# Kernel tuning notes

Hardware: AMD Instinct MI355X
Metric: run time of the kernel (lower is better)

## Reference

```python
import jax, jax.numpy as jnp
import numpy as np

HEAD_NUM = 6

def setup_inputs() -> dict:
    key = jax.random.key(0)
    k1, k2, k3 = jax.random.split(key, 3)
    B, N, P, C = 4, 64, 256, 384
    x = jax.random.normal(k1, (B, N, P, C), dtype=jnp.float32)
    # torch Linear init scale ~ 1/sqrt(fan_in); keep magnitudes sane
    w_qkv = jax.random.normal(k2, (C, 3 * C), dtype=jnp.float32) * (1.0 / np.sqrt(C))
    w_proj = jax.random.normal(k3, (C, C), dtype=jnp.float32) * (1.0 / np.sqrt(C))
    b_proj = jnp.zeros((C,), dtype=jnp.float32)
    return {"x": x, "w_qkv": w_qkv, "w_proj": w_proj, "b_proj": b_proj}

def reference(x, w_qkv, w_proj, b_proj):
    B, N, P, C = x.shape
    H = HEAD_NUM
    D = C // H
    scale = jnp.asarray(D, dtype=x.dtype)  # NOTE: head_dim ** 1, faithful to source
    qkv = (x @ w_qkv).reshape(B, N, P, 3, H, D)
    q = qkv[:, :, :, 0]  # (B, N, P, H, D)
    k = qkv[:, :, :, 1]
    v = qkv[:, :, :, 2]
    attn = jnp.einsum('bnphd,bnqhd->bnhpq', q, k) * scale  # (B,N,H,P,P)
    attn = jax.nn.softmax(attn, axis=-1)
    out = jnp.einsum('bnhpq,bnqhd->bnphd', attn, v).reshape(B, N, P, C)
    return out @ w_proj + b_proj
```

## Files before the change

### kernel.cpp

```cpp
#include <hip/hip_runtime.h>

typedef __bf16 bf16_t;
typedef __bf16 bf16x8 __attribute__((ext_vector_type(8)));
typedef float f32x4 __attribute__((ext_vector_type(4)));
typedef unsigned short u16;
typedef unsigned short u16x4 __attribute__((ext_vector_type(4)));
typedef unsigned int u32;

#define B_ 4
#define N_ 64
#define P_ 256
#define C_ 384
#define H_ 6
#define D_ 64
#define M_TOTAL 65536
#define NQKV 1152
#define KSTEPS 12
#define NFRAG 12
#define WF_HSTRIDE (KSTEPS*NFRAG*512)
#define NBLK (H_*B_*N_)
#define FUSED_LDS 139264
#define PB_STRIDE 40
#define SB() __builtin_amdgcn_sched_barrier(0)

__device__ __forceinline__ u16 f2b(float f){ return __builtin_bit_cast(u16, (bf16_t)f); }
__device__ __forceinline__ f32x4 mfma(bf16x8 a, bf16x8 b, f32x4 c){
    return __builtin_amdgcn_mfma_f32_16x16x32_bf16(a, b, c, 0, 0, 0);
}

__global__ __launch_bounds__(256) void prep_w(
    const float* __restrict__ wqkv, const float* __restrict__ wproj,
    u16* __restrict__ Wfh, u16* __restrict__ Wfl, u16* __restrict__ wPt)
{
    int i = blockIdx.x * 256 + threadIdx.x;
    const int NSLOT = H_ * KSTEPS * NFRAG * 64;
    if (i < NSLOT) {
        int lane = i & 63;
        int frag = i >> 6;
        int nf = frag % NFRAG;
        int ks = (frag / NFRAG) % KSTEPS;
        int h  = frag / (NFRAG * KSTEPS);
        int part = nf >> 2;
        int nh   = (nf & 3) * 16 + (lane & 15);
        int col  = part * C_ + h * 64 + nh;
        int k0   = ks * 32 + (lane >> 4) * 8;
        #pragma unroll
        for (int e = 0; e < 8; ++e) {
            float w = wqkv[(size_t)(k0 + e) * NQKV + col];
            bf16_t hi = (bf16_t)w;
            Wfh[(size_t)i * 8 + e] = __builtin_bit_cast(u16, hi);
            Wfl[(size_t)i * 8 + e] = f2b(w - (float)hi);
        }
    }
    int j = i - NSLOT;
    if (j >= 0 && j < C_ * C_) {
        int k = j / C_, n = j % C_;
        wPt[(size_t)n * C_ + k] = f2b(wproj[j]);
    }
}

__global__ __launch_bounds__(512)
__attribute__((amdgpu_waves_per_eu(2, 2)))
void fused_attn(
    const float* __restrict__ x, const u16* __restrict__ Wfh,
    const u16* __restrict__ Wfl, u16* __restrict__ attn)
{
    extern __shared__ u16 sm[];
    u16* Kh = sm;
    u16* Kl = sm + 16384;
    u16* Vt = sm + 32768;
    u16* Qb = sm + 49152;

    const int tid  = threadIdx.x;
    const int lane = tid & 63, wid = tid >> 6;
    const int g = lane >> 4, r16 = lane & 15;

    const int p = blockIdx.x;
    const int logical = (p & 7) * (NBLK / 8) + (p >> 3);
    const int h  = logical % H_;
    const int bn = logical / H_;
    const size_t row0 = (size_t)bn * P_;
    const int m0w = wid * 32;

    f32x4 acc[2][12];
    #pragma unroll
    for (int mf = 0; mf < 2; ++mf)
        #pragma unroll
        for (int nf = 0; nf < 12; ++nf) acc[mf][nf] = f32x4{0.f,0.f,0.f,0.f};

    const float* xr0 = x + (row0 + m0w + r16) * C_;
    const float* xr1 = xr0 + 16 * C_;
    const u16* wh = Wfh + (size_t)h * WF_HSTRIDE + lane * 8;
    const u16* wl = Wfl + (size_t)h * WF_HSTRIDE + lane * 8;

    bf16x8 bhv[2][12];
    bf16x8 blv[2][8];
    bf16x8 ahq[2][2], alq[2][2];
    f32x4 xr[4];

#define SPLIT_A(par) do {                                                    \
    _Pragma("unroll")                                                        \
    for (int e = 0; e < 4; ++e) {                                            \
        bf16_t h0 = (bf16_t)xr[0][e], h1 = (bf16_t)xr[1][e];                 \
        ahq[par][0][e]   = h0; alq[par][0][e]   = (bf16_t)(xr[0][e] - (float)h0); \
        ahq[par][0][4+e] = h1; alq[par][0][4+e] = (bf16_t)(xr[1][e] - (float)h1); \
        bf16_t h2 = (bf16_t)xr[2][e], h3 = (bf16_t)xr[3][e];                 \
        ahq[par][1][e]   = h2; alq[par][1][e]   = (bf16_t)(xr[2][e] - (float)h2); \
        ahq[par][1][4+e] = h3; alq[par][1][4+e] = (bf16_t)(xr[3][e] - (float)h3); \
    } } while (0)

#define XLOAD(ks_) do {                                                      \
    const float* _xp0 = xr0 + (ks_) * 32 + 8 * g;                            \
    const float* _xp1 = xr1 + (ks_) * 32 + 8 * g;                            \
    xr[0] = *(const f32x4*)_xp0; xr[1] = *(const f32x4*)(_xp0 + 4);          \
    xr[2] = *(const f32x4*)_xp1; xr[3] = *(const f32x4*)(_xp1 + 4);          \
    } while (0)

    XLOAD(0);
    {
        const u16* whk = wh;  const u16* wlk = wl;
        #pragma unroll
        for (int nf = 0; nf < 12; ++nf) bhv[0][nf] = *(const bf16x8*)(whk + nf * 512);
        #pragma unroll
        for (int nf = 0; nf < 8;  ++nf) blv[0][nf] = *(const bf16x8*)(wlk + nf * 512);
    }
    SPLIT_A(0);

    #pragma unroll
    for (int ks = 0; ks < KSTEPS; ++ks) {
        const int par = ks & 1, nxt = par ^ 1;
        const u16* whk1 = wh + (ks + 1) * (NFRAG * 512);
        const u16* wlk1 = wl + (ks + 1) * (NFRAG * 512);

        if (ks < KSTEPS - 1) {
            XLOAD(ks + 1);
            #pragma unroll
            for (int nf = 0; nf < 4; ++nf) bhv[nxt][nf] = *(const bf16x8*)(whk1 + nf * 512);
        }
        SB();
        #pragma unroll
        for (int nf = 0; nf < 4; ++nf) {
            acc[0][nf] = mfma(ahq[par][0], bhv[par][nf], acc[0][nf]);
            acc[1][nf] = mfma(ahq[par][1], bhv[par][nf], acc[1][nf]);
            acc[0][nf] = mfma(ahq[par][0], blv[par][nf], acc[0][nf]);
            acc[1][nf] = mfma(ahq[par][1], blv[par][nf], acc[1][nf]);
            acc[0][nf] = mfma(alq[par][0], bhv[par][nf], acc[0][nf]);
            acc[1][nf] = mfma(alq[par][1], bhv[par][nf], acc[1][nf]);
        }
        SB();
        if (ks < KSTEPS - 1) {
            #pragma unroll
            for (int nf = 0; nf < 4; ++nf) blv[nxt][nf] = *(const bf16x8*)(wlk1 + nf * 512);
            #pragma unroll
            for (int nf = 4; nf < 8; ++nf) bhv[nxt][nf] = *(const bf16x8*)(whk1 + nf * 512);
        }
        SB();
        #pragma unroll
        for (int nf = 4; nf < 8; ++nf) {
            acc[0][nf] = mfma(ahq[par][0], bhv[par][nf], acc[0][nf]);
            acc[1][nf] = mfma(ahq[par][1], bhv[par][nf], acc[1][nf]);
            acc[0][nf] = mfma(ahq[par][0], blv[par][nf], acc[0][nf]);
            acc[1][nf] = mfma(ahq[par][1], blv[par][nf], acc[1][nf]);
            acc[0][nf] = mfma(alq[par][0], bhv[par][nf], acc[0][nf]);
            acc[1][nf] = mfma(alq[par][1], bhv[par][nf], acc[1][nf]);
        }
        SB();
        if (ks < KSTEPS - 1) {
            #pragma unroll
            for (int nf = 4; nf < 8;  ++nf) blv[nxt][nf] = *(const bf16x8*)(wlk1 + nf * 512);
            #pragma unroll
            for (int nf = 8; nf < 12; ++nf) bhv[nxt][nf] = *(const bf16x8*)(whk1 + nf * 512);
            SPLIT_A(nxt);
        }
        SB();
        #pragma unroll
        for (int nf = 8; nf < 12; ++nf) {
            acc[0][nf] = mfma(ahq[par][0], bhv[par][nf], acc[0][nf]);
            acc[1][nf] = mfma(ahq[par][1], bhv[par][nf], acc[1][nf]);
        }
        SB();
    }

    #pragma unroll
    for (int mf = 0; mf < 2; ++mf)
    #pragma unroll
    for (int f = 0; f < 4; ++f)
    #pragma unroll
    for (int rr = 0; rr < 4; ++rr) {
        int q = m0w + mf * 16 + 4 * g + rr;
        int d = f * 16 + r16;
        int ek = q * 64 + (((d >> 3) ^ (q & 7)) << 3) + (d & 7);
        float kv = acc[mf][4 + f][rr];
        bf16_t khi = (bf16_t)kv;
        Kh[ek] = __builtin_bit_cast(u16, khi);
        Kl[ek] = f2b(kv - (float)khi);
        Vt[d * 256 + (((q >> 3) ^ (d & 7)) << 3) + (q & 7)] = f2b(acc[mf][8 + f][rr]);
    }

    u16* myQb = Qb + wid * 2560;
    bf16x8 aqh[2][2], aql[2][2];
    #pragma unroll
    for (int mf = 0; mf < 2; ++mf)
    #pragma unroll
    for (int f = 0; f < 4; ++f)
    #pragma unroll
    for (int rr = 0; rr < 4; ++rr) {
        int r = mf * 16 + 4 * g + rr;
        int c = f * 16 + r16;
        myQb[r * 64 + (((c >> 3) ^ (r & 7)) << 3) + (c & 7)] = f2b(acc[mf][f][rr]);
    }
    #pragma unroll
    for (int mf = 0; mf < 2; ++mf)
    #pragma unroll
    for (int k2 = 0; k2 < 2; ++k2) {
        int r = mf * 16 + r16;
        aqh[mf][k2] = *(const bf16x8*)&myQb[r * 64 + (((k2 * 4 + g) ^ (r & 7)) << 3)];
    }
    SB();
    #pragma unroll
    for (int mf = 0; mf < 2; ++mf)
    #pragma unroll
    for (int f = 0; f < 4; ++f)
    #pragma unroll
    for (int rr = 0; rr < 4; ++rr) {
        int r = mf * 16 + 4 * g + rr;
        int c = f * 16 + r16;
        float v = acc[mf][f][rr];
        bf16_t hi = (bf16_t)v;
        myQb[r * 64 + (((c >> 3) ^ (r & 7)) << 3) + (c & 7)] = f2b(v - (float)hi);
    }
    #pragma unroll
    for (int mf = 0; mf < 2; ++mf)
    #pragma unroll
    for (int k2 = 0; k2 < 2; ++k2) {
        int r = mf * 16 + r16;
        aql[mf][k2] = *(const bf16x8*)&myQb[r * 64 + (((k2 * 4 + g) ^ (r & 7)) << 3)];
    }

    __syncthreads();

    f32x4 S[2][16];
    #pragma unroll
    for (int mf = 0; mf < 2; ++mf)
        #pragma unroll
        for (int nf = 0; nf < 16; ++nf) S[mf][nf] = f32x4{0.f,0.f,0.f,0.f};

    bf16x8 khv[2][2], klv[2][2];
    {
        int q = r16;
        #pragma unroll
        for (int k2 = 0; k2 < 2; ++k2) {
            int e = q * 64 + (((k2 * 4 + g) ^ (q & 7)) << 3);
            khv[0][k2] = *(const bf16x8*)&Kh[e];
            klv[0][k2] = *(const bf16x8*)&Kl[e];
        }
    }
    #pragma unroll
    for (int nf = 0; nf < 16; ++nf) {
        const int par = nf & 1, nxt = par ^ 1;
        if (nf < 15) {
            int q = (nf + 1) * 16 + r16;
            #pragma unroll
            for (int k2 = 0; k2 < 2; ++k2) {
                int e = q * 64 + (((k2 * 4 + g) ^ (q & 7)) << 3);
                khv[nxt][k2] = *(const bf16x8*)&Kh[e];
                klv[nxt][k2] = *(const bf16x8*)&Kl[e];
            }
        }
        SB();
        __builtin_amdgcn_s_setprio(1);
        #pragma unroll
        for (int k2 = 0; k2 < 2; ++k2) {
            S[0][nf] = mfma(aqh[0][k2], khv[par][k2], S[0][nf]);
            S[1][nf] = mfma(aqh[1][k2], khv[par][k2], S[1][nf]);
            S[0][nf] = mfma(aqh[0][k2], klv[par][k2], S[0][nf]);
            S[1][nf] = mfma(aqh[1][k2], klv[par][k2], S[1][nf]);
            S[0][nf] = mfma(aql[0][k2], khv[par][k2], S[0][nf]);
            S[1][nf] = mfma(aql[1][k2], khv[par][k2], S[1][nf]);
        }
        __builtin_amdgcn_s_setprio(0);
        SB();
    }

    float inv_[2][4];
    #pragma unroll
    for (int mf = 0; mf < 2; ++mf) {
        float mrow[4] = {-1e30f,-1e30f,-1e30f,-1e30f};
        #pragma unroll
        for (int nf = 0; nf < 16; ++nf)
            #pragma unroll
            for (int rr = 0; rr < 4; ++rr) mrow[rr] = fmaxf(mrow[rr], S[mf][nf][rr]);
        #pragma unroll
        for (int mask = 1; mask < 16; mask <<= 1)
            #pragma unroll
            for (int rr = 0; rr < 4; ++rr) mrow[rr] = fmaxf(mrow[rr], __shfl_xor(mrow[rr], mask, 64));
        float ssum[4] = {0.f,0.f,0.f,0.f};
        #pragma unroll
        for (int nf = 0; nf < 16; ++nf)
            #pragma unroll
            for (int rr = 0; rr < 4; ++rr) {
                float pv = __expf((S[mf][nf][rr] - mrow[rr]) * 64.0f);
                S[mf][nf][rr] = pv;
                ssum[rr] += pv;
            }
        #pragma unroll
        for (int mask = 1; mask < 16; mask <<= 1)
            #pragma unroll
            for (int rr = 0; rr < 4; ++rr) ssum[rr] += __shfl_xor(ssum[rr], mask, 64);
        #pragma unroll
        for (int rr = 0; rr < 4; ++rr) inv_[mf][rr] = 1.0f / ssum[rr];
    }

    f32x4 O[2][4];
    #pragma unroll
    for (int mf = 0; mf < 2; ++mf)
        #pragma unroll
        for (int f = 0; f < 4; ++f) O[mf][f] = f32x4{0.f,0.f,0.f,0.f};

    bf16x8 bvv[2][4];
    #pragma unroll
    for (int f = 0; f < 4; ++f) {
        int d = f * 16 + r16;
        bvv[0][f] = *(const bf16x8*)&Vt[d * 256 + ((((8 * g) >> 3) ^ (d & 7)) << 3)];
    }
    #pragma unroll
    for (int t = 0; t < 8; ++t) {
        const int par = t & 1, nxt = par ^ 1;
        if (t < 7) {
            #pragma unroll
            for (int f = 0; f < 4; ++f) {
                int d = f * 16 + r16;
                bvv[nxt][f] = *(const bf16x8*)&Vt[d * 256 + (((((t + 1) * 32 + 8 * g) >> 3) ^ (d & 7)) << 3)];
            }
        }
        u16* pb = myQb + par * 1280;
        #pragma unroll
        for (int mf = 0; mf < 2; ++mf)
        #pragma unroll
        for (int tt = 0; tt < 2; ++tt) {
            int nf = 2 * t + tt;
            #pragma unroll
            for (int rr = 0; rr < 4; ++rr)
                pb[(mf * 16 + 4 * g + rr) * PB_STRIDE + tt * 16 + r16] = f2b(S[mf][nf][rr] * inv_[mf][rr]);
        }
        bf16x8 ap0 = *(const bf16x8*)&pb[(r16) * PB_STRIDE + 8 * g];
        bf16x8 ap1 = *(const bf16x8*)&pb[(16 + r16) * PB_STRIDE + 8 * g];
        __builtin_amdgcn_s_setprio(1);
        #pragma unroll
        for (int f = 0; f < 4; ++f) {
            O[0][f] = mfma(ap0, bvv[par][f], O[0][f]);
            O[1][f] = mfma(ap1, bvv[par][f], O[1][f]);
        }
        __builtin_amdgcn_s_setprio(0);
    }

    #pragma unroll
    for (int mf = 0; mf < 2; ++mf)
    #pragma unroll
    for (int f = 0; f < 4; ++f)
    #pragma unroll
    for (int rr = 0; rr < 4; ++rr)
        attn[(row0 + m0w + mf * 16 + 4 * g + rr) * C_ + h * 64 + f * 16 + r16] = f2b(O[mf][f][rr]);
}

__global__ __launch_bounds__(256, 2) void proj_kernel(
    const u16* __restrict__ attn, const u16* __restrict__ wPt,
    const float* __restrict__ bias, float* __restrict__ out)
{
    __shared__ alignas(16) u16 As[128*32];
    __shared__ alignas(16) u16 Bs[128*32];

    const int tid = threadIdx.x;
    const int lane = tid & 63, wid = tid >> 6;
    const int wr = wid >> 1, wc = wid & 1;
    const int g = lane >> 4, r16 = lane & 15;
    const int m0 = blockIdx.x * 128;
    const int n0 = blockIdx.y * 128;

    f32x4 acc[4][4];
    for (int i = 0; i < 4; i++) for (int j = 0; j < 4; j++) acc[i][j] = f32x4{0.f,0.f,0.f,0.f};

    for (int kt = 0; kt < C_; kt += 32) {
        for (int r = 0; r < 4; ++r) {
            int i = tid + 256*r;
            int mm = i >> 3;
            int kk = (i & 7) << 2;
            u16x4 v = *(const u16x4*)&attn[(size_t)(m0+mm)*C_ + kt + kk];
            int e = mm*32 + (((kk>>3) ^ ((mm>>1)&3))<<3) + (kk&7);
            *(u16x4*)&As[e] = v;
        }
        for (int r = 0; r < 4; ++r) {
            int i = tid + 256*r;
            int nn = i >> 3;
            int kk = (i & 7) << 2;
            u16x4 v = *(const u16x4*)&wPt[(size_t)(n0+nn)*C_ + kt + kk];
            int e = nn*32 + (((kk>>3) ^ ((nn>>1)&3))<<3) + (kk&7);
            *(u16x4*)&Bs[e] = v;
        }
        __syncthreads();

        bf16x8 a[4], b[4];
        for (int i = 0; i < 4; i++) {
            int row = wr*64 + i*16 + r16;
            a[i] = *(const bf16x8*)&As[row*32 + ((g ^ ((row>>1)&3))<<3)];
        }
        for (int j = 0; j < 4; j++) {
            int n = wc*64 + j*16 + r16;
            b[j] = *(const bf16x8*)&Bs[n*32 + ((g ^ ((n>>1)&3))<<3)];
        }
        for (int i = 0; i < 4; i++) for (int j = 0; j < 4; j++)
            acc[i][j] = mfma(a[i], b[j], acc[i][j]);
        __syncthreads();
    }

    for (int i = 0; i < 4; i++) for (int j = 0; j < 4; j++) for (int rr = 0; rr < 4; rr++) {
        size_t row = m0 + wr*64 + i*16 + g*4 + rr;
        int col = n0 + wc*64 + j*16 + r16;
        out[row*C_ + col] = acc[i][j][rr] + bias[col];
    }
}

extern "C" void kernel_launch(void* const* d_in, const int* in_sizes, int n_in,
                              void* d_out, int out_size, void* d_ws, size_t ws_size,
                              hipStream_t stream)
{
    const float* x      = (const float*)d_in[0];
    const float* w_qkv  = (const float*)d_in[1];
    const float* w_proj = (const float*)d_in[2];
    const float* b_proj = (const float*)d_in[3];
    float* out = (float*)d_out;

    u16* ws = (u16*)d_ws;
    u16* attnb = ws;
    size_t off = (size_t)M_TOTAL * C_;
    u16* Wfh = ws + off; off += (size_t)H_ * WF_HSTRIDE;
    u16* Wfl = ws + off; off += (size_t)H_ * WF_HSTRIDE;
    u16* wPt = ws + off; off += (size_t)C_ * C_;

    hipFuncSetAttribute((const void*)fused_attn,
                        hipFuncAttributeMaxDynamicSharedMemorySize, FUSED_LDS);

    int prep_n = H_ * KSTEPS * NFRAG * 64 + C_ * C_;
    prep_w<<<dim3((prep_n + 255) / 256), 256, 0, stream>>>(w_qkv, w_proj, Wfh, Wfl, wPt);
    fused_attn<<<dim3(NBLK), 512, FUSED_LDS, stream>>>(x, Wfh, Wfl, attnb);
    proj_kernel<<<dim3(M_TOTAL / 128, C_ / 128), 256, 0, stream>>>(attnb, wPt, b_proj, out);
}
```

Measured before the change: 281.3 us.

## Stage QKV weight fragments through LDS with async global_load_lds double buffering

```diff
diff --git a/kernel.cpp b/kernel.cpp
--- a/kernel.cpp
+++ b/kernel.cpp
@@ -16,12 +16,16 @@
 #define M_TOTAL 65536
 #define NQKV 1152
 #define KSTEPS 12
-#define NFRAG 12
-#define WF_HSTRIDE (KSTEPS*NFRAG*512)
 #define NBLK (H_*B_*N_)
+#define WKS_BYTES 24576
+#define WKS_U16   12288
 #define FUSED_LDS 139264
 #define PB_STRIDE 40
 #define SB() __builtin_amdgcn_sched_barrier(0)
+
+#define GLOAD_LDS16(g, l) __builtin_amdgcn_global_load_lds( \
+    (const __attribute__((address_space(1))) void*)(g), \
+    (__attribute__((address_space(3))) void*)(l), 16, 0, 0)
 
 __device__ __forceinline__ u16 f2b(float f){ return __builtin_bit_cast(u16, (bf16_t)f); }
 __device__ __forceinline__ f32x4 mfma(bf16x8 a, bf16x8 b, f32x4 c){
@@ -30,26 +34,27 @@
 
 __global__ __launch_bounds__(256) void prep_w(
     const float* __restrict__ wqkv, const float* __restrict__ wproj,
-    u16* __restrict__ Wfh, u16* __restrict__ Wfl, u16* __restrict__ wPt)
+    u16* __restrict__ Wpk, u16* __restrict__ wPt)
 {
     int i = blockIdx.x * 256 + threadIdx.x;
-    const int NSLOT = H_ * KSTEPS * NFRAG * 64;
+    const int NSLOT = H_ * KSTEPS * 12 * 64;
     if (i < NSLOT) {
         int lane = i & 63;
         int frag = i >> 6;
-        int nf = frag % NFRAG;
-        int ks = (frag / NFRAG) % KSTEPS;
-        int h  = frag / (NFRAG * KSTEPS);
+        int nf = frag % 12;
+        int ks = (frag / 12) % KSTEPS;
+        int h  = frag / (12 * KSTEPS);
         int part = nf >> 2;
         int nh   = (nf & 3) * 16 + (lane & 15);
         int col  = part * C_ + h * 64 + nh;
         int k0   = ks * 32 + (lane >> 4) * 8;
+        size_t base = (size_t)(h * KSTEPS + ks) * WKS_U16 + nf * 512 + lane * 8;
         #pragma unroll
         for (int e = 0; e < 8; ++e) {
             float w = wqkv[(size_t)(k0 + e) * NQKV + col];
             bf16_t hi = (bf16_t)w;
-            Wfh[(size_t)i * 8 + e] = __builtin_bit_cast(u16, hi);
-            Wfl[(size_t)i * 8 + e] = f2b(w - (float)hi);
+            Wpk[base + e]        = __builtin_bit_cast(u16, hi);
+            Wpk[base + 6144 + e] = f2b(w - (float)hi);
         }
     }
     int j = i - NSLOT;
@@ -59,11 +64,9 @@
     }
 }
 
-__global__ __launch_bounds__(512)
-__attribute__((amdgpu_waves_per_eu(2, 2)))
-void fused_attn(
-    const float* __restrict__ x, const u16* __restrict__ Wfh,
-    const u16* __restrict__ Wfl, u16* __restrict__ attn)
+__global__ __launch_bounds__(512, 2) void fused_attn(
+    const float* __restrict__ x, const u16* __restrict__ Wpk,
+    u16* __restrict__ attn)
 {
     extern __shared__ u16 sm[];
     u16* Kh = sm;
@@ -90,95 +93,67 @@
 
     const float* xr0 = x + (row0 + m0w + r16) * C_;
     const float* xr1 = xr0 + 16 * C_;
-    const u16* wh = Wfh + (size_t)h * WF_HSTRIDE + lane * 8;
-    const u16* wl = Wfl + (size_t)h * WF_HSTRIDE + lane * 8;
-
-    bf16x8 bhv[2][12];
-    bf16x8 blv[2][8];
-    bf16x8 ahq[2][2], alq[2][2];
-    f32x4 xr[4];
-
-#define SPLIT_A(par) do {                                                    \
-    _Pragma("unroll")                                                        \
-    for (int e = 0; e < 4; ++e) {                                            \
-        bf16_t h0 = (bf16_t)xr[0][e], h1 = (bf16_t)xr[1][e];                 \
-        ahq[par][0][e]   = h0; alq[par][0][e]   = (bf16_t)(xr[0][e] - (float)h0); \
-        ahq[par][0][4+e] = h1; alq[par][0][4+e] = (bf16_t)(xr[1][e] - (float)h1); \
-        bf16_t h2 = (bf16_t)xr[2][e], h3 = (bf16_t)xr[3][e];                 \
-        ahq[par][1][e]   = h2; alq[par][1][e]   = (bf16_t)(xr[2][e] - (float)h2); \
-        ahq[par][1][4+e] = h3; alq[par][1][4+e] = (bf16_t)(xr[3][e] - (float)h3); \
+    const char* wbase = (const char*)Wpk + (size_t)h * (KSTEPS * WKS_BYTES);
+
+#define STAGE(ks_, par_) do { \
+    const char* _gp = wbase + (size_t)(ks_) * WKS_BYTES; \
+    char* _lp = (char*)(sm + (par_) * WKS_U16); \
+    GLOAD_LDS16(_gp + tid * 16,          _lp + tid * 16); \
+    GLOAD_LDS16(_gp + 8192 + tid * 16,   _lp + 8192 + tid * 16); \
+    GLOAD_LDS16(_gp + 16384 + tid * 16,  _lp + 16384 + tid * 16); \
+} while (0)
+
+    f32x4 xr[2][4];
+#define XLOAD(ks_, par_) do { \
+    const float* _xp0 = xr0 + (ks_) * 32 + 8 * g; \
+    const float* _xp1 = xr1 + (ks_) * 32 + 8 * g; \
+    xr[par_][0] = *(const f32x4*)_xp0; xr[par_][1] = *(const f32x4*)(_xp0 + 4); \
+    xr[par_][2] = *(const f32x4*)_xp1; xr[par_][3] = *(const f32x4*)(_xp1 + 4); \
+} while (0)
+
+    bf16x8 ah[2], al[2];
+#define SPLIT_A(par_) do { \
+    _Pragma("unroll") \
+    for (int e = 0; e < 4; ++e) { \
+        bf16_t h0 = (bf16_t)xr[par_][0][e], h1 = (bf16_t)xr[par_][1][e]; \
+        ah[0][e]   = h0; al[0][e]   = (bf16_t)(xr[par_][0][e] - (float)h0); \
+        ah[0][4+e] = h1; al[0][4+e] = (bf16_t)(xr[par_][1][e] - (float)h1); \
+        bf16_t h2 = (bf16_t)xr[par_][2][e], h3 = (bf16_t)xr[par_][3][e]; \
+        ah[1][e]   = h2; al[1][e]   = (bf16_t)(xr[par_][2][e] - (float)h2); \
+        ah[1][4+e] = h3; al[1][4+e] = (bf16_t)(xr[par_][3][e] - (float)h3); \
     } } while (0)
 
-#define XLOAD(ks_) do {                                                      \
-    const float* _xp0 = xr0 + (ks_) * 32 + 8 * g;                            \
-    const float* _xp1 = xr1 + (ks_) * 32 + 8 * g;                            \
-    xr[0] = *(const f32x4*)_xp0; xr[1] = *(const f32x4*)(_xp0 + 4);          \
-    xr[2] = *(const f32x4*)_xp1; xr[3] = *(const f32x4*)(_xp1 + 4);          \
-    } while (0)
-
-    XLOAD(0);
-    {
-        const u16* whk = wh;  const u16* wlk = wl;
-        #pragma unroll
-        for (int nf = 0; nf < 12; ++nf) bhv[0][nf] = *(const bf16x8*)(whk + nf * 512);
-        #pragma unroll
-        for (int nf = 0; nf < 8;  ++nf) blv[0][nf] = *(const bf16x8*)(wlk + nf * 512);
-    }
-    SPLIT_A(0);
+    STAGE(0, 0);
+    XLOAD(0, 0);
+    __syncthreads();
 
     #pragma unroll
     for (int ks = 0; ks < KSTEPS; ++ks) {
         const int par = ks & 1, nxt = par ^ 1;
-        const u16* whk1 = wh + (ks + 1) * (NFRAG * 512);
-        const u16* wlk1 = wl + (ks + 1) * (NFRAG * 512);
-
         if (ks < KSTEPS - 1) {
-            XLOAD(ks + 1);
-            #pragma unroll
-            for (int nf = 0; nf < 4; ++nf) bhv[nxt][nf] = *(const bf16x8*)(whk1 + nf * 512);
-        }
-        SB();
-        #pragma unroll
-        for (int nf = 0; nf < 4; ++nf) {
-            acc[0][nf] = mfma(ahq[par][0], bhv[par][nf], acc[0][nf]);
-            acc[1][nf] = mfma(ahq[par][1], bhv[par][nf], acc[1][nf]);
-            acc[0][nf] = mfma(ahq[par][0], blv[par][nf], acc[0][nf]);
-            acc[1][nf] = mfma(ahq[par][1], blv[par][nf], acc[1][nf]);
-            acc[0][nf] = mfma(alq[par][0], bhv[par][nf], acc[0][nf]);
-            acc[1][nf] = mfma(alq[par][1], bhv[par][nf], acc[1][nf]);
-        }
-        SB();
-        if (ks < KSTEPS - 1) {
-            #pragma unroll
-            for (int nf = 0; nf < 4; ++nf) blv[nxt][nf] = *(const bf16x8*)(wlk1 + nf * 512);
-            #pragma unroll
-            for (int nf = 4; nf < 8; ++nf) bhv[nxt][nf] = *(const bf16x8*)(whk1 + nf * 512);
-        }
-        SB();
-        #pragma unroll
-        for (int nf = 4; nf < 8; ++nf) {
-            acc[0][nf] = mfma(ahq[par][0], bhv[par][nf], acc[0][nf]);
-            acc[1][nf] = mfma(ahq[par][1], bhv[par][nf], acc[1][nf]);
-            acc[0][nf] = mfma(ahq[par][0], blv[par][nf], acc[0][nf]);
-            acc[1][nf] = mfma(ahq[par][1], blv[par][nf], acc[1][nf]);
-            acc[0][nf] = mfma(alq[par][0], bhv[par][nf], acc[0][nf]);
-            acc[1][nf] = mfma(alq[par][1], bhv[par][nf], acc[1][nf]);
-        }
-        SB();
-        if (ks < KSTEPS - 1) {
-            #pragma unroll
-            for (int nf = 4; nf < 8;  ++nf) blv[nxt][nf] = *(const bf16x8*)(wlk1 + nf * 512);
-            #pragma unroll
-            for (int nf = 8; nf < 12; ++nf) bhv[nxt][nf] = *(const bf16x8*)(whk1 + nf * 512);
-            SPLIT_A(nxt);
-        }
-        SB();
+            STAGE(ks + 1, nxt);
+            XLOAD(ks + 1, nxt);
+        }
+        SPLIT_A(par);
+        const u16* stg = sm + par * WKS_U16;
+        #pragma unroll
+        for (int nf = 0; nf < 8; ++nf) {
+            bf16x8 bh = *(const bf16x8*)&stg[nf * 512 + lane * 8];
+            bf16x8 bl = *(const bf16x8*)&stg[6144 + nf * 512 + lane * 8];
+            acc[0][nf] = mfma(ah[0], bh, acc[0][nf]);
+            acc[1][nf] = mfma(ah[1], bh, acc[1][nf]);
+            acc[0][nf] = mfma(ah[0], bl, acc[0][nf]);
+            acc[1][nf] = mfma(ah[1], bl, acc[1][nf]);
+            acc[0][nf] = mfma(al[0], bh, acc[0][nf]);
+            acc[1][nf] = mfma(al[1], bh, acc[1][nf]);
+        }
         #pragma unroll
         for (int nf = 8; nf < 12; ++nf) {
-            acc[0][nf] = mfma(ahq[par][0], bhv[par][nf], acc[0][nf]);
-            acc[1][nf] = mfma(ahq[par][1], bhv[par][nf], acc[1][nf]);
-        }
-        SB();
+            bf16x8 bh = *(const bf16x8*)&stg[nf * 512 + lane * 8];
+            acc[0][nf] = mfma(ah[0], bh, acc[0][nf]);
+            acc[1][nf] = mfma(ah[1], bh, acc[1][nf]);
+        }
+        __syncthreads();
     }
 
     #pragma unroll
@@ -433,15 +408,14 @@
     u16* ws = (u16*)d_ws;
     u16* attnb = ws;
     size_t off = (size_t)M_TOTAL * C_;
-    u16* Wfh = ws + off; off += (size_t)H_ * WF_HSTRIDE;
-    u16* Wfl = ws + off; off += (size_t)H_ * WF_HSTRIDE;
+    u16* Wpk = ws + off; off += (size_t)H_ * KSTEPS * WKS_U16;
     u16* wPt = ws + off; off += (size_t)C_ * C_;
 
     hipFuncSetAttribute((const void*)fused_attn,
                         hipFuncAttributeMaxDynamicSharedMemorySize, FUSED_LDS);
 
-    int prep_n = H_ * KSTEPS * NFRAG * 64 + C_ * C_;
-    prep_w<<<dim3((prep_n + 255) / 256), 256, 0, stream>>>(w_qkv, w_proj, Wfh, Wfl, wPt);
-    fused_attn<<<dim3(NBLK), 512, FUSED_LDS, stream>>>(x, Wfh, Wfl, attnb);
+    int prep_n = H_ * KSTEPS * 12 * 64 + C_ * C_;
+    prep_w<<<dim3((prep_n + 255) / 256), 256, 0, stream>>>(w_qkv, w_proj, Wpk, wPt);
+    fused_attn<<<dim3(NBLK), 512, FUSED_LDS, stream>>>(x, Wpk, attnb);
     proj_kernel<<<dim3(M_TOTAL / 128, C_ / 128), 256, 0, stream>>>(attnb, wPt, b_proj, out);
 }
```

Result: faster. 265.6 us (-5.6%).
